# Kernel optimization log

Measured on AMD Instinct MI355X. Metric: run time of the kernel, lower is better.

The kernel has to match this reference:

```python
import jax, jax.numpy as jnp
import numpy as np

N_HEAD = 16
N_KV_HEAD = 4


def setup_inputs() -> dict:
    key = jax.random.key(0)
    ks = jax.random.split(key, 5)
    B, T, C = 2, 2048, 2048
    kv_dim = (C // N_HEAD) * N_KV_HEAD  # 512
    s = 0.02
    return {
        "x": jax.random.normal(ks[0], (B, T, C), dtype=jnp.float32),
        "Wq": jax.random.normal(ks[1], (C, C), dtype=jnp.float32) * s,
        "Wk": jax.random.normal(ks[2], (kv_dim, C), dtype=jnp.float32) * s,
        "Wv": jax.random.normal(ks[3], (kv_dim, C), dtype=jnp.float32) * s,
        "Wo": jax.random.normal(ks[4], (C, C), dtype=jnp.float32) * s,
    }


def reference(x, Wq, Wk, Wv, Wo):
    B, T, C = x.shape
    H, KV = N_HEAD, N_KV_HEAD
    hd = C // H          # 128
    g = H // KV          # query groups per kv head
    scale = hd ** -0.5

    # projections (torch Linear: y = x @ W.T)
    # q heads laid out so head h -> (kv = h // g, group j = h % g),
    # matching repeat_interleave(groups, dim=1) on k/v.
    q = (x @ Wq.T).reshape(B, T, KV, g, hd).transpose(0, 2, 3, 1, 4)  # [B,KV,g,T,hd]
    k = (x @ Wk.T).reshape(B, T, KV, hd).transpose(0, 2, 1, 3)        # [B,KV,T,hd]
    v = (x @ Wv.T).reshape(B, T, KV, hd).transpose(0, 2, 1, 3)        # [B,KV,T,hd]

    # GQA attention without materializing repeated KV heads
    att = jnp.einsum("bkgtd,bksd->bkgts", q, k) * scale  # [B,KV,g,T,T]
    causal = jnp.tril(jnp.ones((T, T), dtype=bool))
    att = jnp.where(causal, att, jnp.float32(-jnp.inf))
    att = jax.nn.softmax(att, axis=-1)
    # dropout p = config.dropout assumed 0 (eval/deterministic reference)

    out = jnp.einsum("bkgts,bksd->bkgtd", att, v)          # [B,KV,g,T,hd]
    out = out.transpose(0, 3, 1, 2, 4).reshape(B, T, C)    # [B,T,C]
    return out @ Wo.T
```

## Files before the change

kernel.cpp:

```cpp
#include <hip/hip_runtime.h>
#include <hip/hip_bf16.h>
#include <math.h>

typedef __bf16 bf16;
typedef __bf16 bf16x4 __attribute__((ext_vector_type(4)));
typedef __bf16 bf16x8 __attribute__((ext_vector_type(8)));
typedef float f32x4 __attribute__((ext_vector_type(4)));
typedef float f32x16 __attribute__((ext_vector_type(16)));
typedef unsigned int uint32x4 __attribute__((ext_vector_type(4)));

__device__ __forceinline__ void gload_lds16(const void* g, void* l) {
  __builtin_amdgcn_global_load_lds(
      (const __attribute__((address_space(1))) void*)g,
      (__attribute__((address_space(3))) void*)l, 16, 0, 0);
}

__device__ __forceinline__ unsigned int packbf(float a, float b) {
  union { bf16 h[2]; unsigned int u; } x;
  x.h[0] = (bf16)a; x.h[1] = (bf16)b;
  return x.u;
}

__global__ void cvt_all(const float* __restrict__ x,  const float* __restrict__ Wq,
                        const float* __restrict__ Wk, const float* __restrict__ Wv,
                        const float* __restrict__ Wo,
                        bf16* __restrict__ xb, bf16* __restrict__ wqkv, bf16* __restrict__ wob,
                        float qscale) {
  const int stride = gridDim.x * blockDim.x;
  const int total4 = 4718592;
  for (int i = blockIdx.x * blockDim.x + threadIdx.x; i < total4; i += stride) {
    const size_t e = (size_t)i * 4;
    const float* src; bf16* dst; size_t off; float sc = 1.f;
    if (e < 8388608)       { src = x;  dst = xb;            off = e; }
    else if (e < 12582912) { src = Wq; dst = wqkv;          off = e - 8388608; sc = qscale; }
    else if (e < 13631488) { src = Wk; dst = wqkv + 4194304; off = e - 12582912; }
    else if (e < 14680064) { src = Wv; dst = wqkv + 5242880; off = e - 13631488; }
    else                   { src = Wo; dst = wob;           off = e - 14680064; }
    float4 v = *(const float4*)(src + off);
    bf16x4 o;
    o[0] = (bf16)(v.x * sc); o[1] = (bf16)(v.y * sc);
    o[2] = (bf16)(v.z * sc); o[3] = (bf16)(v.w * sc);
    *(bf16x4*)(dst + off) = o;
  }
}

__global__ __launch_bounds__(256)
void gemm_qkv(const bf16* __restrict__ A, const bf16* __restrict__ B,
              bf16* __restrict__ Qb, bf16* __restrict__ Kb, bf16* __restrict__ Vtb) {
  const int K = 2048;
  __shared__ __align__(16) char smem[16384];

  const int lane = threadIdx.x & 63;
  const int w    = threadIdx.x >> 6;
  const int wr   = w >> 1, wc = w & 1;
  const int brow = blockIdx.y, bcol = blockIdx.x;

  f32x4 acc[4][4] = {};

  const bf16* Ab = A + (size_t)brow * 128 * K;
  const bf16* Bb = B + (size_t)bcol * 128 * K;

  const int srow = w * 32 + (lane >> 2);
  const int skc  = (lane & 3) * 8;

  for (int k0 = 0; k0 < K; k0 += 32) {
    gload_lds16(Ab + (size_t)srow * K + k0 + skc,        smem + w * 2048);
    gload_lds16(Ab + (size_t)(srow + 16) * K + k0 + skc, smem + w * 2048 + 1024);
    gload_lds16(Bb + (size_t)srow * K + k0 + skc,        smem + 8192 + w * 2048);
    gload_lds16(Bb + (size_t)(srow + 16) * K + k0 + skc, smem + 8192 + w * 2048 + 1024);
    __syncthreads();

    bf16x8 af[4], bfr[4];
#pragma unroll
    for (int i = 0; i < 4; ++i) {
      af[i]  = *(const bf16x8*)(smem + ((wr * 64 + i * 16 + (lane & 15)) * 64 + (lane >> 4) * 16));
      bfr[i] = *(const bf16x8*)(smem + 8192 + ((wc * 64 + i * 16 + (lane & 15)) * 64 + (lane >> 4) * 16));
    }
#pragma unroll
    for (int mi = 0; mi < 4; ++mi)
#pragma unroll
      for (int ni = 0; ni < 4; ++ni)
        acc[mi][ni] = __builtin_amdgcn_mfma_f32_16x16x32_bf16(af[mi], bfr[ni], acc[mi][ni], 0, 0, 0);
    __syncthreads();
  }

  const int r0 = brow * 128 + wr * 64 + (lane >> 4) * 4;
  const int c0 = bcol * 128 + wc * 64 + (lane & 15);
#pragma unroll
  for (int mi = 0; mi < 4; ++mi)
#pragma unroll
    for (int ni = 0; ni < 4; ++ni)
#pragma unroll
      for (int j = 0; j < 4; ++j) {
        const int r = r0 + mi * 16 + j, c = c0 + ni * 16;
        const bf16 v = (bf16)acc[mi][ni][j];
        if (bcol < 16)       Qb[(size_t)r * 2048 + c] = v;
        else if (bcol < 20)  Kb[(size_t)r * 512 + (c - 2048)] = v;
        else                 Vtb[(size_t)(c - 2560) * 4096 + r] = v;
      }
}

__global__ __launch_bounds__(256)
void gemm_nt(const bf16* __restrict__ A, const bf16* __restrict__ B,
             float* __restrict__ C, int M, int N, int K) {
  __shared__ __align__(16) char smem[16384];

  const int lane = threadIdx.x & 63;
  const int w    = threadIdx.x >> 6;
  const int wr   = w >> 1, wc = w & 1;
  const int brow = blockIdx.y, bcol = blockIdx.x;

  f32x4 acc[4][4] = {};

  const bf16* Ab = A + (size_t)brow * 128 * K;
  const bf16* Bb = B + (size_t)bcol * 128 * K;

  const int srow = w * 32 + (lane >> 2);
  const int skc  = (lane & 3) * 8;

  for (int k0 = 0; k0 < K; k0 += 32) {
    gload_lds16(Ab + (size_t)srow * K + k0 + skc,        smem + w * 2048);
    gload_lds16(Ab + (size_t)(srow + 16) * K + k0 + skc, smem + w * 2048 + 1024);
    gload_lds16(Bb + (size_t)srow * K + k0 + skc,        smem + 8192 + w * 2048);
    gload_lds16(Bb + (size_t)(srow + 16) * K + k0 + skc, smem + 8192 + w * 2048 + 1024);
    __syncthreads();

    bf16x8 af[4], bfr[4];
#pragma unroll
    for (int i = 0; i < 4; ++i) {
      af[i]  = *(const bf16x8*)(smem + ((wr * 64 + i * 16 + (lane & 15)) * 64 + (lane >> 4) * 16));
      bfr[i] = *(const bf16x8*)(smem + 8192 + ((wc * 64 + i * 16 + (lane & 15)) * 64 + (lane >> 4) * 16));
    }
#pragma unroll
    for (int mi = 0; mi < 4; ++mi)
#pragma unroll
      for (int ni = 0; ni < 4; ++ni)
        acc[mi][ni] = __builtin_amdgcn_mfma_f32_16x16x32_bf16(af[mi], bfr[ni], acc[mi][ni], 0, 0, 0);
    __syncthreads();
  }

  const int r0 = brow * 128 + wr * 64 + (lane >> 4) * 4;
  const int c0 = bcol * 128 + wc * 64 + (lane & 15);
#pragma unroll
  for (int mi = 0; mi < 4; ++mi)
#pragma unroll
    for (int ni = 0; ni < 4; ++ni)
#pragma unroll
      for (int j = 0; j < 4; ++j)
        C[(size_t)(r0 + mi * 16 + j) * N + c0 + ni * 16] = acc[mi][ni][j];
}

__global__ __launch_bounds__(256, 2)
void attn_fwd(const bf16* __restrict__ Q, const bf16* __restrict__ Kg_,
              const bf16* __restrict__ Vt, bf16* __restrict__ AO) {
  const int T = 2048, C = 2048, KVD = 512, MTOK = 4096;
  const int bid = blockIdx.x;
  const int qt  = (bid < 256) ? (15 - (bid >> 5)) : ((bid >> 5) - 8);
  const int sub = bid & 31;
  const int h = sub & 15, b = sub >> 4;
  const int kvh = h >> 2;
  const int lane = threadIdx.x & 63, w = threadIdx.x >> 6;
  const int hi = lane >> 5, lo = lane & 31;

  __shared__ __align__(16) char smem[65536];
  char* sK  = smem;
  char* sVt = smem + 32768;

  const bf16* Qg = Q   + (size_t)b * T * C + (size_t)h * 128;
  const bf16* Kg = Kg_ + (size_t)b * T * KVD + (size_t)kvh * 128;
  const bf16* Vg = Vt  + (size_t)kvh * 128 * MTOK + (size_t)b * T;

  const int q0 = qt * 128;
  const int qw = q0 + w * 32;

  bf16x8 qf[8];
#pragma unroll
  for (int ks = 0; ks < 8; ++ks)
    qf[ks] = *(const bf16x8*)(Qg + (size_t)(qw + lo) * C + ks * 16 + hi * 8);

  f32x16 ot[4] = {};
  float mstat = -INFINITY, lstat = 0.f;

  const int nt = 2 * qt + 2;

  auto stage = [&](int t, int buf) {
#pragma unroll
    for (int i = 0; i < 4; ++i) {
      const int ci = i * 256 + threadIdx.x;
      const int rk = ci >> 4, ck = ci & 15;
      gload_lds16(Kg + (size_t)(t * 64 + rk) * KVD + ((ck ^ (rk & 7)) * 8),
                  sK + buf * 16384 + i * 4096 + w * 1024);
      const int rv = ci >> 3, cv = ci & 7;
      gload_lds16(Vg + (size_t)rv * MTOK + t * 64 + ((cv ^ (rv & 7)) * 8),
                  sVt + buf * 16384 + i * 4096 + w * 1024);
    }
  };

  auto compute = [&](int t, int buf) {
    const int kv0 = t * 64;
    if (kv0 > qw + 31) return;
    const char* kb = sK + buf * 16384;
    const char* vb = sVt + buf * 16384;

    f32x16 sa[2] = {};
    __builtin_amdgcn_s_setprio(1);
#pragma unroll
    for (int ks = 0; ks < 8; ++ks) {
#pragma unroll
      for (int nb = 0; nb < 2; ++nb) {
        const int r = nb * 32 + lo;
        bf16x8 kf = *(const bf16x8*)(kb + (r * 256 + (((ks * 2 + hi) ^ (r & 7)) * 16)));
        sa[nb] = __builtin_amdgcn_mfma_f32_32x32x16_bf16(kf, qf[ks], sa[nb], 0, 0, 0);
      }
    }
    __builtin_amdgcn_s_setprio(0);
    if (kv0 + 63 > qw) {
      const int qg = qw + lo;
#pragma unroll
      for (int nb = 0; nb < 2; ++nb)
#pragma unroll
        for (int r = 0; r < 16; ++r) {
          const int kvg = kv0 + nb * 32 + (r & 3) + 8 * (r >> 2) + 4 * hi;
          if (kvg > qg) sa[nb][r] = -1e30f;
        }
    }
    float pm = -INFINITY;
#pragma unroll
    for (int nb = 0; nb < 2; ++nb)
#pragma unroll
      for (int r = 0; r < 16; ++r) pm = fmaxf(pm, sa[nb][r]);
    pm = fmaxf(pm, __shfl_xor(pm, 32));

    if (__any(pm > mstat + 8.f)) {
      const float mn = fmaxf(mstat, pm);
      const float rs = __expf(mstat - mn);
      mstat = mn;
      lstat *= rs;
#pragma unroll
      for (int db = 0; db < 4; ++db)
#pragma unroll
        for (int r = 0; r < 16; ++r) ot[db][r] *= rs;
    }

    float ls = 0.f;
    unsigned int pw[2][8];
#pragma unroll
    for (int nb = 0; nb < 2; ++nb)
#pragma unroll
      for (int j = 0; j < 8; ++j) {
        const float e0 = __expf(sa[nb][2 * j]     - mstat);
        const float e1 = __expf(sa[nb][2 * j + 1] - mstat);
        ls += e0 + e1;
        pw[nb][j] = packbf(e0, e1);
      }
    ls += __shfl_xor(ls, 32);
    lstat += ls;

#pragma unroll
    for (int nb = 0; nb < 2; ++nb) {
      unsigned int pj[8];
#pragma unroll
      for (int j = 0; j < 8; ++j) pj[j] = __shfl_xor(pw[nb][j], 32);
      __builtin_amdgcn_s_setprio(1);
#pragma unroll
      for (int half = 0; half < 2; ++half) {
        const int x = half * 4;
        uint32x4 bw;
        bw[0] = hi ? pj[x + 2] : pw[nb][x + 0];
        bw[1] = hi ? pj[x + 3] : pw[nb][x + 1];
        bw[2] = hi ? pw[nb][x + 2] : pj[x + 0];
        bw[3] = hi ? pw[nb][x + 3] : pj[x + 1];
        const bf16x8 pb = __builtin_bit_cast(bf16x8, bw);
        const int ks = nb * 2 + half;
#pragma unroll
        for (int db = 0; db < 4; ++db) {
          const int rv = db * 32 + lo;
          bf16x8 vf = *(const bf16x8*)(vb + (rv * 128 + (((ks * 2 + hi) ^ (rv & 7)) * 16)));
          ot[db] = __builtin_amdgcn_mfma_f32_32x32x16_bf16(vf, pb, ot[db], 0, 0, 0);
        }
      }
      __builtin_amdgcn_s_setprio(0);
    }
  };

  stage(0, 0);
  for (int t = 0; t < nt - 1; ++t) {
    stage(t + 1, (t + 1) & 1);
    asm volatile("s_waitcnt vmcnt(8)" ::: "memory");
    __builtin_amdgcn_s_barrier();
    compute(t, t & 1);
    __builtin_amdgcn_s_barrier();
  }
  asm volatile("s_waitcnt vmcnt(0)" ::: "memory");
  __builtin_amdgcn_s_barrier();
  compute(nt - 1, (nt - 1) & 1);

  __syncthreads();
  char* sO = smem;
  const float inv = 1.f / lstat;
  const int lq = w * 32 + lo;
#pragma unroll
  for (int db = 0; db < 4; ++db) {
#pragma unroll
    for (int j = 0; j < 8; ++j) {
      const int r = 2 * j;
      const int d = db * 32 + (r & 3) + 8 * (r >> 2) + 4 * hi;
      const unsigned int pv = packbf(ot[db][r] * inv, ot[db][r + 1] * inv);
      *(unsigned int*)(sO + (lq * 256 + ((2 * d) ^ (16 * (lq & 7))))) = pv;
    }
  }
  __syncthreads();
  bf16* Og = AO + (size_t)b * T * C + (size_t)h * 128;
#pragma unroll
  for (int i = 0; i < 8; ++i) {
    const int cid = i * 256 + threadIdx.x;
    const int rq = cid >> 4, c = cid & 15;
    bf16x8 vv = *(const bf16x8*)(sO + (rq * 256 + ((c * 16) ^ (16 * (rq & 7)))));
    *(bf16x8*)(Og + (size_t)(q0 + rq) * C + c * 8) = vv;
  }
}

extern "C" void kernel_launch(void* const* d_in, const int* in_sizes, int n_in,
                              void* d_out, int out_size, void* d_ws, size_t ws_size,
                              hipStream_t stream) {
  const int B = 2, T = 2048, C = 2048;
  const int M = B * T;

  const float* x  = (const float*)d_in[0];
  const float* Wq = (const float*)d_in[1];
  const float* Wk = (const float*)d_in[2];
  const float* Wv = (const float*)d_in[3];
  const float* Wo = (const float*)d_in[4];
  float* out = (float*)d_out;

  char* ws = (char*)d_ws;
  bf16* xb   = (bf16*)(ws);
  bf16* wqkv = (bf16*)(ws + 16777216);
  bf16* wob  = (bf16*)(ws + 29360128);
  bf16* Qb   = (bf16*)(ws + 37748736);
  bf16* Kb   = (bf16*)(ws + 54525952);
  bf16* Vtb  = (bf16*)(ws + 58720256);
  bf16* AOb  = (bf16*)(ws + 62914560);

  const float scale = 0.08838834764831845f;
  cvt_all<<<2048, 256, 0, stream>>>(x, Wq, Wk, Wv, Wo, xb, wqkv, wob, scale);

  gemm_qkv<<<dim3(24, 32), 256, 0, stream>>>(xb, wqkv, Qb, Kb, Vtb);

  attn_fwd<<<512, 256, 0, stream>>>(Qb, Kb, Vtb, AOb);

  gemm_nt<<<dim3(C / 128, M / 128), 256, 0, stream>>>(AOb, wob, out, M, C, C);
}
```

Measured before the change: 204.9 us.

## Replace 128x128 GEMMs with double-buffered 256x256 swizzled-LDS GEMM kernel

```diff
diff --git a/kernel.cpp b/kernel.cpp
--- a/kernel.cpp
+++ b/kernel.cpp
@@ -44,110 +44,156 @@
   }
 }
 
-__global__ __launch_bounds__(256)
-void gemm_qkv(const bf16* __restrict__ A, const bf16* __restrict__ B,
-              bf16* __restrict__ Qb, bf16* __restrict__ Kb, bf16* __restrict__ Vtb) {
-  const int K = 2048;
-  __shared__ __align__(16) char smem[16384];
-
-  const int lane = threadIdx.x & 63;
-  const int w    = threadIdx.x >> 6;
-  const int wr   = w >> 1, wc = w & 1;
+template <int MODE>
+__global__ __launch_bounds__(512, 2)
+void gemm256(const bf16* __restrict__ A, const bf16* __restrict__ B,
+             float* __restrict__ Cf, bf16* __restrict__ Qb, bf16* __restrict__ Kb,
+             bf16* __restrict__ Vtb, int K, int Nst) {
+  __shared__ __align__(16) char sA[65536];
+  __shared__ __align__(16) char sB[65536];
+
+  const int tid  = threadIdx.x;
+  const int lane = tid & 63, w = tid >> 6;
+  const int wr   = w >> 2, wc = w & 3;
+  const int fr   = lane & 15, fq = lane >> 4;
   const int brow = blockIdx.y, bcol = blockIdx.x;
 
-  f32x4 acc[4][4] = {};
-
-  const bf16* Ab = A + (size_t)brow * 128 * K;
-  const bf16* Bb = B + (size_t)bcol * 128 * K;
-
-  const int srow = w * 32 + (lane >> 2);
-  const int skc  = (lane & 3) * 8;
-
-  for (int k0 = 0; k0 < K; k0 += 32) {
-    gload_lds16(Ab + (size_t)srow * K + k0 + skc,        smem + w * 2048);
-    gload_lds16(Ab + (size_t)(srow + 16) * K + k0 + skc, smem + w * 2048 + 1024);
-    gload_lds16(Bb + (size_t)srow * K + k0 + skc,        smem + 8192 + w * 2048);
-    gload_lds16(Bb + (size_t)(srow + 16) * K + k0 + skc, smem + 8192 + w * 2048 + 1024);
-    __syncthreads();
-
-    bf16x8 af[4], bfr[4];
+  f32x4 acc[8][4] = {};
+
+  const bf16* Ab = A + (size_t)brow * 256 * K;
+  const bf16* Bb = B + (size_t)bcol * 256 * K;
+
+  const int NT = K >> 6;
+
+  auto stage = [&](int t, int bf) {
 #pragma unroll
     for (int i = 0; i < 4; ++i) {
-      af[i]  = *(const bf16x8*)(smem + ((wr * 64 + i * 16 + (lane & 15)) * 64 + (lane >> 4) * 16));
-      bfr[i] = *(const bf16x8*)(smem + 8192 + ((wc * 64 + i * 16 + (lane & 15)) * 64 + (lane >> 4) * 16));
-    }
+      const int ci = i * 512 + tid;
+      const int r = ci >> 3, ck = ci & 7;
+      const int src = (ck ^ (r & 7)) * 8;
+      gload_lds16(Ab + (size_t)r * K + t * 64 + src, sA + bf * 32768 + i * 8192 + w * 1024);
+      gload_lds16(Bb + (size_t)r * K + t * 64 + src, sB + bf * 32768 + i * 8192 + w * 1024);
+    }
+  };
+
+  stage(0, 0);
+  for (int t = 0; t < NT; ++t) {
+    const int bf = t & 1;
+    if (t + 1 < NT) {
+      stage(t + 1, bf ^ 1);
+      asm volatile("s_waitcnt vmcnt(8)" ::: "memory");
+    } else {
+      asm volatile("s_waitcnt vmcnt(0)" ::: "memory");
+    }
+    __builtin_amdgcn_s_barrier();
+
+    const char* pA = sA + bf * 32768;
+    const char* pB = sB + bf * 32768;
+    bf16x8 af[4][2], bfr[2][2];
+
+#pragma unroll
+    for (int mi = 0; mi < 4; ++mi) {
+      const int r = wr * 128 + mi * 16 + fr;
+#pragma unroll
+      for (int ks = 0; ks < 2; ++ks)
+        af[mi][ks] = *(const bf16x8*)(pA + r * 128 + (((ks * 4 + fq) ^ (r & 7)) * 16));
+    }
+#pragma unroll
+    for (int ni = 0; ni < 2; ++ni) {
+      const int r = wc * 64 + ni * 16 + fr;
+#pragma unroll
+      for (int ks = 0; ks < 2; ++ks)
+        bfr[ni][ks] = *(const bf16x8*)(pB + r * 128 + (((ks * 4 + fq) ^ (r & 7)) * 16));
+    }
+    __builtin_amdgcn_s_barrier();
+    __builtin_amdgcn_s_setprio(1);
 #pragma unroll
     for (int mi = 0; mi < 4; ++mi)
 #pragma unroll
-      for (int ni = 0; ni < 4; ++ni)
-        acc[mi][ni] = __builtin_amdgcn_mfma_f32_16x16x32_bf16(af[mi], bfr[ni], acc[mi][ni], 0, 0, 0);
-    __syncthreads();
-  }
-
-  const int r0 = brow * 128 + wr * 64 + (lane >> 4) * 4;
-  const int c0 = bcol * 128 + wc * 64 + (lane & 15);
-#pragma unroll
-  for (int mi = 0; mi < 4; ++mi)
+      for (int ni = 0; ni < 2; ++ni)
+#pragma unroll
+        for (int ks = 0; ks < 2; ++ks)
+          acc[mi][ni] = __builtin_amdgcn_mfma_f32_16x16x32_bf16(af[mi][ks], bfr[ni][ks], acc[mi][ni], 0, 0, 0);
+    __builtin_amdgcn_s_setprio(0);
+    __builtin_amdgcn_s_barrier();
+
+#pragma unroll
+    for (int ni = 0; ni < 2; ++ni) {
+      const int r = wc * 64 + 32 + ni * 16 + fr;
+#pragma unroll
+      for (int ks = 0; ks < 2; ++ks)
+        bfr[ni][ks] = *(const bf16x8*)(pB + r * 128 + (((ks * 4 + fq) ^ (r & 7)) * 16));
+    }
+    __builtin_amdgcn_s_barrier();
+    __builtin_amdgcn_s_setprio(1);
+#pragma unroll
+    for (int mi = 0; mi < 4; ++mi)
+#pragma unroll
+      for (int ni = 0; ni < 2; ++ni)
+#pragma unroll
+        for (int ks = 0; ks < 2; ++ks)
+          acc[mi][2 + ni] = __builtin_amdgcn_mfma_f32_16x16x32_bf16(af[mi][ks], bfr[ni][ks], acc[mi][2 + ni], 0, 0, 0);
+    __builtin_amdgcn_s_setprio(0);
+    __builtin_amdgcn_s_barrier();
+
+#pragma unroll
+    for (int mi = 0; mi < 4; ++mi) {
+      const int r = wr * 128 + 64 + mi * 16 + fr;
+#pragma unroll
+      for (int ks = 0; ks < 2; ++ks)
+        af[mi][ks] = *(const bf16x8*)(pA + r * 128 + (((ks * 4 + fq) ^ (r & 7)) * 16));
+    }
+    __builtin_amdgcn_s_barrier();
+    __builtin_amdgcn_s_setprio(1);
+#pragma unroll
+    for (int mi = 0; mi < 4; ++mi)
+#pragma unroll
+      for (int ni = 0; ni < 2; ++ni)
+#pragma unroll
+        for (int ks = 0; ks < 2; ++ks)
+          acc[4 + mi][2 + ni] = __builtin_amdgcn_mfma_f32_16x16x32_bf16(af[mi][ks], bfr[ni][ks], acc[4 + mi][2 + ni], 0, 0, 0);
+    __builtin_amdgcn_s_setprio(0);
+    __builtin_amdgcn_s_barrier();
+
+#pragma unroll
+    for (int ni = 0; ni < 2; ++ni) {
+      const int r = wc * 64 + ni * 16 + fr;
+#pragma unroll
+      for (int ks = 0; ks < 2; ++ks)
+        bfr[ni][ks] = *(const bf16x8*)(pB + r * 128 + (((ks * 4 + fq) ^ (r & 7)) * 16));
+    }
+    __builtin_amdgcn_s_barrier();
+    __builtin_amdgcn_s_setprio(1);
+#pragma unroll
+    for (int mi = 0; mi < 4; ++mi)
+#pragma unroll
+      for (int ni = 0; ni < 2; ++ni)
+#pragma unroll
+        for (int ks = 0; ks < 2; ++ks)
+          acc[4 + mi][ni] = __builtin_amdgcn_mfma_f32_16x16x32_bf16(af[mi][ks], bfr[ni][ks], acc[4 + mi][ni], 0, 0, 0);
+    __builtin_amdgcn_s_setprio(0);
+    __builtin_amdgcn_s_barrier();
+  }
+
+  const int r0 = brow * 256 + wr * 128 + fq * 4;
+  const int c0 = bcol * 256 + wc * 64 + fr;
+#pragma unroll
+  for (int mi = 0; mi < 8; ++mi)
 #pragma unroll
     for (int ni = 0; ni < 4; ++ni)
 #pragma unroll
       for (int j = 0; j < 4; ++j) {
-        const int r = r0 + mi * 16 + j, c = c0 + ni * 16;
-        const bf16 v = (bf16)acc[mi][ni][j];
-        if (bcol < 16)       Qb[(size_t)r * 2048 + c] = v;
-        else if (bcol < 20)  Kb[(size_t)r * 512 + (c - 2048)] = v;
-        else                 Vtb[(size_t)(c - 2560) * 4096 + r] = v;
+        const int r = r0 + mi * 16 + j;
+        const int c = c0 + ni * 16;
+        const float v = acc[mi][ni][j];
+        if constexpr (MODE == 0) {
+          Cf[(size_t)r * Nst + c] = v;
+        } else {
+          if (c < 2048)       Qb[(size_t)r * 2048 + c] = (bf16)v;
+          else if (c < 2560)  Kb[(size_t)r * 512 + (c - 2048)] = (bf16)v;
+          else                Vtb[(size_t)(c - 2560) * 4096 + r] = (bf16)v;
+        }
       }
-}
-
-__global__ __launch_bounds__(256)
-void gemm_nt(const bf16* __restrict__ A, const bf16* __restrict__ B,
-             float* __restrict__ C, int M, int N, int K) {
-  __shared__ __align__(16) char smem[16384];
-
-  const int lane = threadIdx.x & 63;
-  const int w    = threadIdx.x >> 6;
-  const int wr   = w >> 1, wc = w & 1;
-  const int brow = blockIdx.y, bcol = blockIdx.x;
-
-  f32x4 acc[4][4] = {};
-
-  const bf16* Ab = A + (size_t)brow * 128 * K;
-  const bf16* Bb = B + (size_t)bcol * 128 * K;
-
-  const int srow = w * 32 + (lane >> 2);
-  const int skc  = (lane & 3) * 8;
-
-  for (int k0 = 0; k0 < K; k0 += 32) {
-    gload_lds16(Ab + (size_t)srow * K + k0 + skc,        smem + w * 2048);
-    gload_lds16(Ab + (size_t)(srow + 16) * K + k0 + skc, smem + w * 2048 + 1024);
-    gload_lds16(Bb + (size_t)srow * K + k0 + skc,        smem + 8192 + w * 2048);
-    gload_lds16(Bb + (size_t)(srow + 16) * K + k0 + skc, smem + 8192 + w * 2048 + 1024);
-    __syncthreads();
-
-    bf16x8 af[4], bfr[4];
-#pragma unroll
-    for (int i = 0; i < 4; ++i) {
-      af[i]  = *(const bf16x8*)(smem + ((wr * 64 + i * 16 + (lane & 15)) * 64 + (lane >> 4) * 16));
-      bfr[i] = *(const bf16x8*)(smem + 8192 + ((wc * 64 + i * 16 + (lane & 15)) * 64 + (lane >> 4) * 16));
-    }
-#pragma unroll
-    for (int mi = 0; mi < 4; ++mi)
-#pragma unroll
-      for (int ni = 0; ni < 4; ++ni)
-        acc[mi][ni] = __builtin_amdgcn_mfma_f32_16x16x32_bf16(af[mi], bfr[ni], acc[mi][ni], 0, 0, 0);
-    __syncthreads();
-  }
-
-  const int r0 = brow * 128 + wr * 64 + (lane >> 4) * 4;
-  const int c0 = bcol * 128 + wc * 64 + (lane & 15);
-#pragma unroll
-  for (int mi = 0; mi < 4; ++mi)
-#pragma unroll
-    for (int ni = 0; ni < 4; ++ni)
-#pragma unroll
-      for (int j = 0; j < 4; ++j)
-        C[(size_t)(r0 + mi * 16 + j) * N + c0 + ni * 16] = acc[mi][ni][j];
 }
 
 __global__ __launch_bounds__(256, 2)
@@ -323,9 +369,6 @@
 extern "C" void kernel_launch(void* const* d_in, const int* in_sizes, int n_in,
                               void* d_out, int out_size, void* d_ws, size_t ws_size,
                               hipStream_t stream) {
-  const int B = 2, T = 2048, C = 2048;
-  const int M = B * T;
-
   const float* x  = (const float*)d_in[0];
   const float* Wq = (const float*)d_in[1];
   const float* Wk = (const float*)d_in[2];
@@ -345,9 +388,9 @@
   const float scale = 0.08838834764831845f;
   cvt_all<<<2048, 256, 0, stream>>>(x, Wq, Wk, Wv, Wo, xb, wqkv, wob, scale);
 
-  gemm_qkv<<<dim3(24, 32), 256, 0, stream>>>(xb, wqkv, Qb, Kb, Vtb);
+  gemm256<1><<<dim3(12, 16), 512, 0, stream>>>(xb, wqkv, nullptr, Qb, Kb, Vtb, 2048, 0);
 
   attn_fwd<<<512, 256, 0, stream>>>(Qb, Kb, Vtb, AOb);
 
-  gemm_nt<<<dim3(C / 128, M / 128), 256, 0, stream>>>(AOb, wob, out, M, C, C);
-}
+  gemm256<0><<<dim3(8, 16), 512, 0, stream>>>(AOb, wob, out, nullptr, nullptr, nullptr, 2048, 2048);
+}
```

Result: slower. 255.7 us (+24.8%).
